# Kernel tuning notes

Measured on AMD Instinct MI355X. Metric: run time of the kernel, lower is better.

## Reference

```python
import jax, jax.numpy as jnp
import numpy as np

ENC_DIM = 512
B, T = 2048, 256
NUM_PARTS, PART_DIM, ATT_DIM, VOCAB = 64, 32, 128, 12


def _p(key, shape, scale=0.05):
    return jax.random.normal(key, shape, dtype=jnp.float32) * scale


def setup_inputs() -> dict:
    key = jax.random.key(0)
    ks = jax.random.split(key, 24)
    inp = {
        "img_features": jax.random.normal(ks[0], (B, 32, 8, 8), dtype=jnp.float32),
        "label": jax.random.normal(ks[1], (B, T, VOCAB), dtype=jnp.float32),
        # Attention params
        "Ww": _p(ks[2], (ATT_DIM, PART_DIM)), "Wb": _p(ks[3], (ATT_DIM,)),
        "Uw": _p(ks[4], (ATT_DIM, ENC_DIM)), "Ub": _p(ks[5], (ATT_DIM,)),
        "vw": _p(ks[6], (1, ATT_DIM)), "vb": _p(ks[7], (1,)),
        "betaw": _p(ks[8], (PART_DIM, ENC_DIM)), "betab": _p(ks[9], (PART_DIM,)),
        # init hidden params
        "ihw": _p(ks[10], (ENC_DIM, NUM_PARTS)), "ihb": _p(ks[11], (ENC_DIM,)),
        "icw": _p(ks[12], (ENC_DIM, NUM_PARTS)), "icb": _p(ks[13], (ENC_DIM,)),
        # LSTMCell params (PyTorch layout: [4*H, in] / [4*H, H])
        "W_ih": _p(ks[14], (4 * ENC_DIM, VOCAB + PART_DIM)),
        "W_hh": _p(ks[15], (4 * ENC_DIM, ENC_DIM)),
        "b_ih": _p(ks[16], (4 * ENC_DIM,)), "b_hh": _p(ks[17], (4 * ENC_DIM,)),
        # output fc
        "ow": _p(ks[18], (VOCAB, ENC_DIM)), "ob": _p(ks[19], (VOCAB,)),
    }
    return inp


def reference(img_features, label, Ww, Wb, Uw, Ub, vw, vb, betaw, betab,
              ihw, ihb, icw, icb, W_ih, W_hh, b_ih, b_hh, ow, ob):
    b = img_features.shape[0]
    feats = img_features.reshape(b, 32, -1)          # [B, 32, 64]
    parts = feats.transpose(0, 2, 1)                  # [B, 64, 32]
    # init hidden/cell from mean over channel dim (dim=1 in torch)
    avg = feats.mean(axis=1)                          # [B, 64]
    h0 = jnp.tanh(avg @ ihw.T + ihb)                  # [B, H]
    c0 = jnp.tanh(avg @ icw.T + icb)
    # W_s depends only on img features: hoist out of the loop (same math)
    Ws = parts @ Ww.T + Wb                            # [B, 64, 128]
    lab = label.transpose(1, 0, 2)                    # [T, B, 12]

    H = h0.shape[1]

    def step(carry, x_t):
        h, c = carry
        Uh = h @ Uw.T + Ub                            # [B, 128]
        att = jnp.tanh(Ws + Uh[:, None, :])           # [B, 64, 128]
        score = (att @ vw.T + vb)[..., 0]             # [B, 64]
        alpha = jax.nn.softmax(score, axis=1)
        ctx = jnp.einsum('bp,bpd->bd', alpha, parts)  # [B, 32]
        beta = jax.nn.sigmoid(h @ betaw.T + betab)
        ctx = ctx * beta
        inp = jnp.concatenate([x_t, ctx], axis=1)     # [B, 44]
        gates = inp @ W_ih.T + b_ih + h @ W_hh.T + b_hh
        i, f, g, o = jnp.split(gates, 4, axis=1)
        c2 = jax.nn.sigmoid(f) * c + jax.nn.sigmoid(i) * jnp.tanh(g)
        h2 = jax.nn.sigmoid(o) * jnp.tanh(c2)
        out = h2 @ ow.T + ob                          # [B, 12]
        return (h2, c2), (out, alpha)

    (_, _), (outs, alphas) = jax.lax.scan(step, (h0, c0), lab)
    output = jax.nn.log_softmax(outs, axis=-1).transpose(1, 0, 2)  # [B, T, 12]
    return output, alphas  # alphas: [T, B, 64] (stacked version of the list)
```

## Files before the change

kernel.cpp:

```cpp
#include <hip/hip_runtime.h>
#include <hip/hip_bf16.h>


typedef __attribute__((ext_vector_type(8))) short short8;
typedef __attribute__((ext_vector_type(4))) float floatx4;

#define DEV static __device__ __forceinline__
#define C2LE 2.885390082f
#define LOG2E 1.4426950409f
#define LN2 0.6931471806f

DEV unsigned short f2bf(float f) {
    unsigned int u = __float_as_uint(f);
    unsigned int r = (u + 0x7FFFu + ((u >> 16) & 1u)) >> 16;
    return (unsigned short)r;
}
DEV float bf2f(unsigned short u) { return __uint_as_float(((unsigned int)u) << 16); }
DEV float rcp_f(float x) { float r; asm("v_rcp_f32 %0, %1" : "=v"(r) : "v"(x)); return r; }
DEV float tanh_f(float x) { return 1.f - 2.f * rcp_f(1.f + exp2f(x * C2LE)); }
DEV float sigm(float x) { return rcp_f(1.f + exp2f(-x * LOG2E)); }

DEV void ldg16_sc(short8* d, const unsigned short* p) {
    asm volatile("global_load_dwordx4 %0, %1, off sc0 sc1" : "=v"(*d) : "v"(p));
}
DEV void stg2_sc(unsigned short* p, unsigned short v) {
    unsigned int vv = v;
    asm volatile("global_store_short %0, %1, off sc0 sc1" :: "v"(p), "v"(vv) : "memory");
}
DEV void st_flag(int* p, int v) {
    asm volatile("global_store_dword %0, %1, off sc0 sc1" :: "v"(p), "v"(v) : "memory");
}
DEV int ld_flag(const int* p) {
    int v;
    asm volatile("global_load_dword %0, %1, off sc0 sc1\n\ts_waitcnt vmcnt(0)"
                 : "=v"(v) : "v"(p) : "memory");
    return v;
}

#define OFF_XH0    ((size_t)0)
#define OFF_XH1    ((size_t)2359296)
#define OFF_C0     ((size_t)4718592)
#define OFF_PARTS  ((size_t)8912896)
#define OFF_WBIG   ((size_t)17301504)
#define OFF_WSMALL ((size_t)19660800)
#define OFF_WW2    ((size_t)19824640)
#define OFF_BIAS   ((size_t)19832832)
#define OFF_AVG    ((size_t)19841024)
#define OFF_FLAGS  ((size_t)20365312)

DEV void gbar(int* flags, int bk, int g16, int step) {
    asm volatile("s_waitcnt vmcnt(0)" ::: "memory");
    __syncthreads();
    if (threadIdx.x < 64) {
        int lane = threadIdx.x;
        if (lane == 0) st_flag(flags + bk * 32, step);
        for (;;) {
            int v = step;
            if (lane < 16) v = ld_flag(flags + (g16 + lane) * 32);
            if (__all(v >= step)) break;
            __builtin_amdgcn_s_sleep(1);
        }
    }
    __syncthreads();
}

__global__ void k_init(int* flags) {
    int i = blockIdx.x * 256 + threadIdx.x;
    if (i < 256 * 32) flags[i] = 0;
}

__global__ void k_avg(const float* __restrict__ img, float* __restrict__ avg) {
    int idx = blockIdx.x * 256 + threadIdx.x;
    int b = idx >> 6, p = idx & 63;
    const float* base = img + (size_t)b * 2048 + p;
    float s = 0.f;
#pragma unroll
    for (int k = 0; k < 32; ++k) s += base[k * 64];
    avg[idx] = s * (1.f / 32.f);
}

__global__ void k_prep(const float* __restrict__ Whh, const float* __restrict__ Wih,
                       const float* __restrict__ Uw, const float* __restrict__ betaw,
                       const float* __restrict__ Ww, const float* __restrict__ bih,
                       const float* __restrict__ bhh,
                       unsigned short* __restrict__ Wbig, unsigned short* __restrict__ Wsmall,
                       unsigned short* __restrict__ Ww2, float* __restrict__ bias_cat) {
    int p = blockIdx.x, tid = threadIdx.x;
    int g = p & 3, j = p >> 2, orig = g * 512 + j;
    for (int k = tid; k < 576; k += 256) {
        float v = 0.f;
        if (k < 512) v = Whh[(size_t)orig * 512 + k];
        else if (k < 556) v = Wih[(size_t)orig * 44 + (k - 512)];
        Wbig[(size_t)p * 576 + k] = f2bf(v);
    }
    if (p < 160) {
        for (int k = tid; k < 512; k += 256) {
            float v = (p < 128) ? Uw[(size_t)p * 512 + k] : betaw[(size_t)(p - 128) * 512 + k];
            Wsmall[(size_t)p * 512 + k] = f2bf(v);
        }
    }
    if (p < 128 && tid < 32) Ww2[p * 32 + tid] = f2bf(C2LE * Ww[p * 32 + tid]);
    if (tid == 0) bias_cat[orig] = bih[orig] + bhh[orig];
}

__global__ __launch_bounds__(512) void k_h0c0(const float* __restrict__ avg,
                                              const float* __restrict__ ihw, const float* __restrict__ ihb,
                                              const float* __restrict__ icw, const float* __restrict__ icb,
                                              unsigned short* __restrict__ xh0, unsigned short* __restrict__ xh1,
                                              float* __restrict__ c0) {
    __shared__ float avg_s[8][64];
    int b0 = blockIdx.x * 8, tid = threadIdx.x;
    for (int i = tid; i < 8 * 64; i += 512) avg_s[i >> 6][i & 63] = avg[b0 * 64 + i];
    __syncthreads();
    int j = tid;
    float w0[64];
#pragma unroll
    for (int p4 = 0; p4 < 16; ++p4) {
        float4 v = ((const float4*)(ihw + j * 64))[p4];
        w0[p4 * 4 + 0] = v.x; w0[p4 * 4 + 1] = v.y; w0[p4 * 4 + 2] = v.z; w0[p4 * 4 + 3] = v.w;
    }
    float bh = ihb[j];
#pragma unroll
    for (int bb = 0; bb < 8; ++bb) {
        float s = bh;
#pragma unroll
        for (int p = 0; p < 64; ++p) s += w0[p] * avg_s[bb][p];
        xh0[(size_t)(b0 + bb) * 576 + j] = f2bf(tanh_f(s));
        if (j < 20) {
            xh0[(size_t)(b0 + bb) * 576 + 556 + j] = 0;
            xh1[(size_t)(b0 + bb) * 576 + 556 + j] = 0;
        }
    }
#pragma unroll
    for (int p4 = 0; p4 < 16; ++p4) {
        float4 v = ((const float4*)(icw + j * 64))[p4];
        w0[p4 * 4 + 0] = v.x; w0[p4 * 4 + 1] = v.y; w0[p4 * 4 + 2] = v.z; w0[p4 * 4 + 3] = v.w;
    }
    float bc = icb[j];
#pragma unroll
    for (int bb = 0; bb < 8; ++bb) {
        float s = bc;
#pragma unroll
        for (int p = 0; p < 64; ++p) s += w0[p] * avg_s[bb][p];
        c0[(size_t)(b0 + bb) * 512 + j] = tanh_f(s);
    }
}

__global__ __launch_bounds__(256) void k_parts(const float* __restrict__ img,
                                               unsigned short* __restrict__ parts_bf) {
    __shared__ float pl[64][33];
    int b = blockIdx.x, tid = threadIdx.x;
    const float* ib = img + (size_t)b * 2048;
    for (int i = tid; i < 2048; i += 256) pl[i & 63][i >> 6] = ib[i];
    __syncthreads();
    for (int i = tid; i < 2048; i += 256)
        parts_bf[(size_t)b * 2048 + i] = f2bf(pl[i >> 5][i & 31]);
}

__global__ __launch_bounds__(512, 2) void k_scan(
    unsigned short* __restrict__ xh0, unsigned short* __restrict__ xh1,
    const float* __restrict__ c0,
    const unsigned short* __restrict__ parts_bf,
    const unsigned short* __restrict__ Wsmall, const unsigned short* __restrict__ Wbig,
    const unsigned short* __restrict__ Ww2, const float* __restrict__ bias_cat,
    const float* __restrict__ Ub, const float* __restrict__ betab, const float* __restrict__ Wb,
    const float* __restrict__ vw,
    const float* __restrict__ label, const float* __restrict__ ow, const float* __restrict__ ob,
    float* __restrict__ out_alpha, float* __restrict__ out_logits,
    int* __restrict__ flags)
{
    __shared__ unsigned short Ald[128 * 584];
    __shared__ float uh_l[8][160];
    __shared__ float al_l[8][64];
    __shared__ float vw2_l[128];
    __shared__ float bias_sl[128];

    const int tid = threadIdx.x, w = tid >> 6, lane = tid & 63;
    const int bk = blockIdx.x;
    const int mtile = bk >> 4, ntile = bk & 15;
    const int g16 = mtile * 16;
    const int wm = w >> 2, wn = w & 3;

    if (tid < 128) {
        vw2_l[tid] = -2.f * vw[tid];
        bias_sl[tid] = bias_cat[(tid >> 5) * 512 + ntile * 32 + (tid & 31)];
    }
    float creg[32];
#pragma unroll
    for (int mf = 0; mf < 4; ++mf)
#pragma unroll
        for (int nf = 0; nf < 2; ++nf)
#pragma unroll
            for (int r = 0; r < 4; ++r) {
                int b = mtile * 128 + wm * 64 + mf * 16 + (lane >> 4) * 4 + r;
                int j = ntile * 32 + wn * 8 + nf * 4 + (lane & 3);
                creg[(mf * 2 + nf) * 4 + r] = c0[(size_t)b * 512 + j];
            }
    __syncthreads();
    float vwsum = 0.f;
#pragma unroll
    for (int d = 0; d < 128; ++d) vwsum += vw2_l[d];
    vwsum *= -0.5f;

    auto stage_A = [&](const unsigned short* xin) {
#pragma unroll
        for (int half = 0; half < 2; ++half) {
            short8 tmp[9];
#pragma unroll
            for (int q = 0; q < 9; ++q) {
                int cid = tid + (half * 9 + q) * 512;
                int row = cid / 72, c16 = cid % 72;
                ldg16_sc(&tmp[q], xin + (size_t)(mtile * 128 + row) * 576 + c16 * 8);
            }
            asm volatile("s_waitcnt vmcnt(0)" ::: "memory");
            __builtin_amdgcn_sched_barrier(0);
#pragma unroll
            for (int q = 0; q < 9; ++q) {
                int cid = tid + (half * 9 + q) * 512;
                int row = cid / 72, c16 = cid % 72;
                *(short8*)&Ald[row * 584 + c16 * 8] = tmp[q];
            }
        }
    };

    auto phase1 = [&](unsigned short* xout) {
        const unsigned short* Bp = Wbig + (size_t)(ntile * 128 + wn * 32 + (lane & 15)) * 576 + (lane >> 4) * 8;
        const unsigned short* Ab = &Ald[(wm * 64 + (lane & 15)) * 584 + (lane >> 4) * 8];
        floatx4 acc[4][2] = {};
#pragma unroll 3
        for (int kk = 0; kk < 18; ++kk) {
            int k0 = kk * 32;
            short8 b0 = *(const short8*)(Bp + k0);
            short8 b1 = *(const short8*)(Bp + 16 * 576 + k0);
#pragma unroll
            for (int mf = 0; mf < 4; ++mf) {
                short8 a = *(const short8*)(Ab + mf * 16 * 584 + k0);
                acc[mf][0] = __builtin_amdgcn_mfma_f32_16x16x32_bf16(a, b0, acc[mf][0], 0, 0, 0);
                acc[mf][1] = __builtin_amdgcn_mfma_f32_16x16x32_bf16(a, b1, acc[mf][1], 0, 0, 0);
            }
        }
        int base = (lane & 48) | (4 * (lane & 3));
        int jl = wn * 8 + (lane & 3);
#pragma unroll
        for (int mf = 0; mf < 4; ++mf)
#pragma unroll
            for (int nf = 0; nf < 2; ++nf) {
#pragma unroll
                for (int r = 0; r < 4; ++r) {
                    float x = acc[mf][nf][r];
                    float g0 = __shfl(x, base + 0);
                    float g1 = __shfl(x, base + 1);
                    float g2 = __shfl(x, base + 2);
                    float g3 = __shfl(x, base + 3);
                    int jj = jl + nf * 4;
                    float gi = g0 + bias_sl[jj];
                    float gf = g1 + bias_sl[32 + jj];
                    float gg = g2 + bias_sl[64 + jj];
                    float go = g3 + bias_sl[96 + jj];
                    int ci = (mf * 2 + nf) * 4 + r;
                    float c2 = sigm(gf) * creg[ci] + sigm(gi) * tanh_f(gg);
                    creg[ci] = c2;
                    float h2 = sigm(go) * tanh_f(c2);
                    if (((lane >> 2) & 3) == 0) {
                        int bg = mtile * 128 + wm * 64 + mf * 16 + (lane >> 4) * 4 + r;
                        stg2_sc(xout + (size_t)bg * 576 + ntile * 32 + jj, f2bf(h2));
                    }
                }
            }
    };

    auto phase2 = [&](int tt, unsigned short* xb, bool do_head, bool do_attn) {
        {
            int row = tid >> 6, c16 = tid & 63;
            short8 tv;
            ldg16_sc(&tv, xb + (size_t)(bk * 8 + row) * 576 + c16 * 8);
            asm volatile("s_waitcnt vmcnt(0)" ::: "memory");
            __builtin_amdgcn_sched_barrier(0);
            *(short8*)&Ald[(ntile * 8 + row) * 584 + c16 * 8] = tv;
        }
        __syncthreads();
        int b = bk * 8 + w;
        if (do_head) {
            short8 hv = *(const short8*)&Ald[(ntile * 8 + w) * 584 + lane * 8];
            float hf[8];
#pragma unroll
            for (int j = 0; j < 8; ++j) hf[j] = bf2f((unsigned short)hv[j]);
            float ov[12];
#pragma unroll
            for (int v = 0; v < 12; ++v) {
                const float* owr = ow + v * 512 + lane * 8;
                float4 o0 = *(const float4*)owr;
                float4 o1 = *(const float4*)(owr + 4);
                float p = hf[0] * o0.x + hf[1] * o0.y + hf[2] * o0.z + hf[3] * o0.w
                        + hf[4] * o1.x + hf[5] * o1.y + hf[6] * o1.z + hf[7] * o1.w;
#pragma unroll
                for (int o = 32; o; o >>= 1) p += __shfl_xor(p, o);
                ov[v] = p + ob[v];
            }
            float mx = ov[0];
#pragma unroll
            for (int v = 1; v < 12; ++v) mx = fmaxf(mx, ov[v]);
            float ss = 0.f;
#pragma unroll
            for (int v = 0; v < 12; ++v) ss += exp2f((ov[v] - mx) * LOG2E);
            float lse = mx + log2f(ss) * LN2;
#pragma unroll
            for (int v = 0; v < 12; ++v)
                if (lane == v) out_logits[((size_t)b * 256 + (tt - 1)) * 12 + v] = ov[v] - lse;
        }
        if (do_attn && w < 5) {
            const unsigned short* Bp = Wsmall + (size_t)(w * 32 + (lane & 15)) * 512 + (lane >> 4) * 8;
            const unsigned short* Ab = &Ald[(ntile * 8 + (lane & 7)) * 584 + (lane >> 4) * 8];
            floatx4 u0 = {}, u1 = {};
#pragma unroll 4
            for (int k0 = 0; k0 < 512; k0 += 32) {
                short8 a = *(const short8*)(Ab + k0);
                u0 = __builtin_amdgcn_mfma_f32_16x16x32_bf16(a, *(const short8*)(Bp + k0), u0, 0, 0, 0);
                u1 = __builtin_amdgcn_mfma_f32_16x16x32_bf16(a, *(const short8*)(Bp + 16 * 512 + k0), u1, 0, 0, 0);
            }
            int r0 = (lane >> 4) * 4, cc = lane & 15;
            if (r0 < 8) {
#pragma unroll
                for (int q = 0; q < 2; ++q) {
                    int n = w * 32 + q * 16 + cc;
#pragma unroll
                    for (int r = 0; r < 4; ++r) {
                        float val = (q ? u1[r] : u0[r]);
                        uh_l[r0 + r][n] = (n < 128) ? C2LE * (val + Ub[n] + Wb[n])
                                                    : (val + betab[n - 128]);
                    }
                }
            }
        }
        __syncthreads();
        if (do_attn) {
            const unsigned short* pb = parts_bf + (size_t)b * 2048;
            short8 pa[4];
#pragma unroll
            for (int mt = 0; mt < 4; ++mt)
                pa[mt] = *(const short8*)(pb + ((lane & 15) + 16 * mt) * 32 + (lane >> 4) * 8);
            float sc[4][4] = {};
#pragma unroll
            for (int nt = 0; nt < 8; ++nt) {
                short8 wwf = *(const short8*)(Ww2 + (size_t)((lane & 15) + 16 * nt) * 32 + (lane >> 4) * 8);
                int d = nt * 16 + (lane & 15);
                float ud = uh_l[w][d];
                float v2 = vw2_l[d];
#pragma unroll
                for (int mt = 0; mt < 4; ++mt) {
                    floatx4 z = {};
                    floatx4 wsa = __builtin_amdgcn_mfma_f32_16x16x32_bf16(pa[mt], wwf, z, 0, 0, 0);
#pragma unroll
                    for (int r = 0; r < 4; ++r)
                        sc[mt][r] += v2 * rcp_f(1.f + exp2f(wsa[r] + ud));
                }
            }
            float mx = -1e30f;
#pragma unroll
            for (int mt = 0; mt < 4; ++mt)
#pragma unroll
                for (int r = 0; r < 4; ++r) {
                    float s = sc[mt][r];
                    s += __shfl_xor(s, 1); s += __shfl_xor(s, 2);
                    s += __shfl_xor(s, 4); s += __shfl_xor(s, 8);
                    s += vwsum;
                    sc[mt][r] = s;
                    mx = fmaxf(mx, s);
                }
            mx = fmaxf(mx, __shfl_xor(mx, 16));
            mx = fmaxf(mx, __shfl_xor(mx, 32));
            float ssum = 0.f;
            float av[4][4];
#pragma unroll
            for (int mt = 0; mt < 4; ++mt)
#pragma unroll
                for (int r = 0; r < 4; ++r) {
                    av[mt][r] = exp2f((sc[mt][r] - mx) * LOG2E);
                    ssum += av[mt][r];
                }
            ssum += __shfl_xor(ssum, 16);
            ssum += __shfl_xor(ssum, 32);
            float rs = rcp_f(ssum);
#pragma unroll
            for (int mt = 0; mt < 4; ++mt) {
                if ((lane & 15) == mt) {
                    float4 fv = make_float4(av[mt][0] * rs, av[mt][1] * rs, av[mt][2] * rs, av[mt][3] * rs);
                    int p0 = mt * 16 + (lane >> 4) * 4;
                    *(float4*)&out_alpha[((size_t)tt * 2048 + b) * 64 + p0] = fv;
                    *(float4*)&al_l[w][p0] = fv;
                }
            }
            int k = lane & 31, half = lane >> 5;
            float cp = 0.f;
#pragma unroll
            for (int p = 0; p < 32; ++p) {
                int pp = half * 32 + p;
                cp += al_l[w][pp] * bf2f(parts_bf[(size_t)b * 2048 + pp * 32 + k]);
            }
            cp += __shfl_xor(cp, 32);
            if (half == 0) {
                float beta = sigm(uh_l[w][128 + k]);
                stg2_sc(xb + (size_t)b * 576 + 524 + k, f2bf(cp * beta));
            }
            if (lane < 12)
                stg2_sc(xb + (size_t)b * 576 + 512 + lane, f2bf(label[((size_t)b * 256 + tt) * 12 + lane]));
        }
    };

    int bc = 0;
    phase2(0, xh0, false, true);
    gbar(flags, bk, g16, ++bc);
    for (int t = 0; t < 256; ++t) {
        const unsigned short* xin = (t & 1) ? xh1 : xh0;
        unsigned short* xout = (t & 1) ? xh0 : xh1;
        stage_A(xin);
        __syncthreads();
        phase1(xout);
        gbar(flags, bk, g16, ++bc);
        phase2(t + 1, xout, true, t < 255);
        if (t < 255) gbar(flags, bk, g16, ++bc);
    }
}

extern "C" void kernel_launch(void* const* d_in, const int* in_sizes, int n_in,
                              void* d_out, int out_size, void* d_ws, size_t ws_size,
                              hipStream_t stream) {
    const float* img   = (const float*)d_in[0];
    const float* label = (const float*)d_in[1];
    const float* Ww    = (const float*)d_in[2];
    const float* Wb    = (const float*)d_in[3];
    const float* Uw    = (const float*)d_in[4];
    const float* Ub    = (const float*)d_in[5];
    const float* vw    = (const float*)d_in[6];
    const float* betaw = (const float*)d_in[8];
    const float* betab = (const float*)d_in[9];
    const float* ihw   = (const float*)d_in[10];
    const float* ihb   = (const float*)d_in[11];
    const float* icw   = (const float*)d_in[12];
    const float* icb   = (const float*)d_in[13];
    const float* Wih   = (const float*)d_in[14];
    const float* Whh   = (const float*)d_in[15];
    const float* bih   = (const float*)d_in[16];
    const float* bhh   = (const float*)d_in[17];
    const float* ow    = (const float*)d_in[18];
    const float* ob    = (const float*)d_in[19];

    char* ws = (char*)d_ws;
    unsigned short* xh0      = (unsigned short*)(ws + OFF_XH0);
    unsigned short* xh1      = (unsigned short*)(ws + OFF_XH1);
    float*          c0       = (float*)(ws + OFF_C0);
    unsigned short* parts_bf = (unsigned short*)(ws + OFF_PARTS);
    unsigned short* Wbig     = (unsigned short*)(ws + OFF_WBIG);
    unsigned short* Wsmall   = (unsigned short*)(ws + OFF_WSMALL);
    unsigned short* Ww2      = (unsigned short*)(ws + OFF_WW2);
    float*          bias     = (float*)(ws + OFF_BIAS);
    float*          avg      = (float*)(ws + OFF_AVG);
    int*            flags    = (int*)(ws + OFF_FLAGS);

    float* out_logits = (float*)d_out;
    float* out_alpha  = out_logits + (size_t)2048 * 256 * 12;

    k_init<<<32, 256, 0, stream>>>(flags);
    k_avg<<<512, 256, 0, stream>>>(img, avg);
    k_prep<<<2048, 256, 0, stream>>>(Whh, Wih, Uw, betaw, Ww, bih, bhh, Wbig, Wsmall, Ww2, bias);
    k_h0c0<<<256, 512, 0, stream>>>(avg, ihw, ihb, icw, icb, xh0, xh1, c0);
    k_parts<<<2048, 256, 0, stream>>>(img, parts_bf);

    k_scan<<<256, 512, 0, stream>>>(xh0, xh1, c0, parts_bf, Wsmall, Wbig, Ww2, bias,
                                    Ub, betab, Wb, vw, label, ow, ob,
                                    out_alpha, out_logits, flags);
}
```

Before: 16.31 ms.

## Retile persistent LSTM scan into 4-block groups with single hidden buffer and LDS caching

Changes the scan tiling from 16 N-tiles per 128-row M-tile to 4 N-tiles per 32-row M-tile. Each inter-block barrier now waits on 4 peers instead of 16. The ping-pong hidden buffers are merged into one, and parts, the output weights and the biases are cached in LDS so they are not reloaded every step. Staging of peer rows is overlapped with the attention computation, and the h and context stores are packed into 8-byte writes. The trade-off is that each block now carries a heavier per-step GEMM (8 N-fragments per wave), and reusing a single buffer relies on carefully ordered barriers to avoid read/write races.

Result: faster. 15.22 ms (-6.7%).

```diff
diff --git a/kernel.cpp b/kernel.cpp
--- a/kernel.cpp
+++ b/kernel.cpp
@@ -4,6 +4,7 @@
 
 typedef __attribute__((ext_vector_type(8))) short short8;
 typedef __attribute__((ext_vector_type(4))) float floatx4;
+typedef __attribute__((ext_vector_type(2))) unsigned int uint2v;
 
 #define DEV static __device__ __forceinline__
 #define C2LE 2.885390082f
@@ -23,9 +24,8 @@
 DEV void ldg16_sc(short8* d, const unsigned short* p) {
     asm volatile("global_load_dwordx4 %0, %1, off sc0 sc1" : "=v"(*d) : "v"(p));
 }
-DEV void stg2_sc(unsigned short* p, unsigned short v) {
-    unsigned int vv = v;
-    asm volatile("global_store_short %0, %1, off sc0 sc1" :: "v"(p), "v"(vv) : "memory");
+DEV void stg8_sc(unsigned short* p, uint2v v) {
+    asm volatile("global_store_dwordx2 %0, %1, off sc0 sc1" :: "v"(p), "v"(v) : "memory");
 }
 DEV void st_flag(int* p, int v) {
     asm volatile("global_store_dword %0, %1, off sc0 sc1" :: "v"(p), "v"(v) : "memory");
@@ -36,27 +36,27 @@
                  : "=v"(v) : "v"(p) : "memory");
     return v;
 }
-
-#define OFF_XH0    ((size_t)0)
-#define OFF_XH1    ((size_t)2359296)
-#define OFF_C0     ((size_t)4718592)
-#define OFF_PARTS  ((size_t)8912896)
-#define OFF_WBIG   ((size_t)17301504)
-#define OFF_WSMALL ((size_t)19660800)
-#define OFF_WW2    ((size_t)19824640)
-#define OFF_BIAS   ((size_t)19832832)
-#define OFF_AVG    ((size_t)19841024)
-#define OFF_FLAGS  ((size_t)20365312)
-
-DEV void gbar(int* flags, int bk, int g16, int step) {
-    asm volatile("s_waitcnt vmcnt(0)" ::: "memory");
+DEV void waitv0() { asm volatile("s_waitcnt vmcnt(0)" ::: "memory"); }
+
+#define OFF_XH     ((size_t)0)
+#define OFF_C0     ((size_t)2359296)
+#define OFF_PARTS  ((size_t)6553600)
+#define OFF_WBIG   ((size_t)14942208)
+#define OFF_WSMALL ((size_t)17301504)
+#define OFF_WW2    ((size_t)17465344)
+#define OFF_BIAS   ((size_t)17473536)
+#define OFF_AVG    ((size_t)17481728)
+#define OFF_FLAGS  ((size_t)18006016)
+
+DEV void gbar(int* flags, int bk, int g4, int step) {
+    waitv0();
     __syncthreads();
     if (threadIdx.x < 64) {
         int lane = threadIdx.x;
         if (lane == 0) st_flag(flags + bk * 32, step);
         for (;;) {
             int v = step;
-            if (lane < 16) v = ld_flag(flags + (g16 + lane) * 32);
+            if (lane < 4) v = ld_flag(flags + (g4 + lane) * 32);
             if (__all(v >= step)) break;
             __builtin_amdgcn_s_sleep(1);
         }
@@ -106,8 +106,7 @@
 __global__ __launch_bounds__(512) void k_h0c0(const float* __restrict__ avg,
                                               const float* __restrict__ ihw, const float* __restrict__ ihb,
                                               const float* __restrict__ icw, const float* __restrict__ icb,
-                                              unsigned short* __restrict__ xh0, unsigned short* __restrict__ xh1,
-                                              float* __restrict__ c0) {
+                                              unsigned short* __restrict__ xh, float* __restrict__ c0) {
     __shared__ float avg_s[8][64];
     int b0 = blockIdx.x * 8, tid = threadIdx.x;
     for (int i = tid; i < 8 * 64; i += 512) avg_s[i >> 6][i & 63] = avg[b0 * 64 + i];
@@ -125,11 +124,8 @@
         float s = bh;
 #pragma unroll
         for (int p = 0; p < 64; ++p) s += w0[p] * avg_s[bb][p];
-        xh0[(size_t)(b0 + bb) * 576 + j] = f2bf(tanh_f(s));
-        if (j < 20) {
-            xh0[(size_t)(b0 + bb) * 576 + 556 + j] = 0;
-            xh1[(size_t)(b0 + bb) * 576 + 556 + j] = 0;
-        }
+        xh[(size_t)(b0 + bb) * 576 + j] = f2bf(tanh_f(s));
+        if (j < 20) xh[(size_t)(b0 + bb) * 576 + 556 + j] = 0;
     }
 #pragma unroll
     for (int p4 = 0; p4 < 16; ++p4) {
@@ -158,7 +154,7 @@
 }
 
 __global__ __launch_bounds__(512, 2) void k_scan(
-    unsigned short* __restrict__ xh0, unsigned short* __restrict__ xh1,
+    unsigned short* __restrict__ xh,
     const float* __restrict__ c0,
     const unsigned short* __restrict__ parts_bf,
     const unsigned short* __restrict__ Wsmall, const unsigned short* __restrict__ Wbig,
@@ -169,146 +165,69 @@
     float* __restrict__ out_alpha, float* __restrict__ out_logits,
     int* __restrict__ flags)
 {
-    __shared__ unsigned short Ald[128 * 584];
+    __shared__ unsigned short Ald[32 * 584];
+    __shared__ unsigned short parts_l[8][2304];
+    __shared__ unsigned short ow_l[12][512];
     __shared__ float uh_l[8][160];
     __shared__ float al_l[8][64];
+    __shared__ float bias_l[512];
+    __shared__ unsigned short xscr[8][48];
     __shared__ float vw2_l[128];
-    __shared__ float bias_sl[128];
+    __shared__ float obl[12];
 
     const int tid = threadIdx.x, w = tid >> 6, lane = tid & 63;
     const int bk = blockIdx.x;
-    const int mtile = bk >> 4, ntile = bk & 15;
-    const int g16 = mtile * 16;
+    const int mtile = bk >> 2, ntile = bk & 3;
+    const int g4 = bk & ~3;
     const int wm = w >> 2, wn = w & 3;
 
-    if (tid < 128) {
-        vw2_l[tid] = -2.f * vw[tid];
-        bias_sl[tid] = bias_cat[(tid >> 5) * 512 + ntile * 32 + (tid & 31)];
+    if (tid < 128) vw2_l[tid] = -2.f * vw[tid];
+    if (tid < 12) obl[tid] = ob[tid];
+    if (tid < 512) {
+        int g = tid >> 7, jl = tid & 127;
+        bias_l[tid] = bias_cat[g * 512 + ntile * 128 + jl];
+    }
+    for (int i = tid; i < 12 * 512; i += 512) ow_l[i >> 9][i & 511] = f2bf(ow[i]);
+    {
+        int row = tid >> 6, p = tid & 63;
+        const short8* src = (const short8*)(parts_bf + (size_t)(bk * 8 + row) * 2048 + p * 32);
+        short8* dst = (short8*)&parts_l[row][p * 36];
+        dst[0] = src[0]; dst[1] = src[1]; dst[2] = src[2]; dst[3] = src[3];
     }
     float creg[32];
 #pragma unroll
-    for (int mf = 0; mf < 4; ++mf)
-#pragma unroll
-        for (int nf = 0; nf < 2; ++nf)
-#pragma unroll
-            for (int r = 0; r < 4; ++r) {
-                int b = mtile * 128 + wm * 64 + mf * 16 + (lane >> 4) * 4 + r;
-                int j = ntile * 32 + wn * 8 + nf * 4 + (lane & 3);
-                creg[(mf * 2 + nf) * 4 + r] = c0[(size_t)b * 512 + j];
-            }
+    for (int nf = 0; nf < 8; ++nf)
+#pragma unroll
+        for (int r = 0; r < 4; ++r) {
+            int b = mtile * 32 + wm * 16 + (lane >> 4) * 4 + r;
+            int j = ntile * 128 + wn * 32 + nf * 4 + (lane & 3);
+            creg[nf * 4 + r] = c0[(size_t)b * 512 + j];
+        }
+    {
+        short8 tv[4];
+#pragma unroll
+        for (int q = 0; q < 4; ++q) {
+            int cid = tid + q * 512;
+            int row = cid >> 6, c16 = cid & 63;
+            ldg16_sc(&tv[q], xh + (size_t)(mtile * 32 + row) * 576 + c16 * 8);
+        }
+        waitv0();
+        __builtin_amdgcn_sched_barrier(0);
+#pragma unroll
+        for (int q = 0; q < 4; ++q) {
+            int cid = tid + q * 512;
+            int row = cid >> 6, c16 = cid & 63;
+            *(short8*)&Ald[row * 584 + c16 * 8] = tv[q];
+        }
+    }
     __syncthreads();
     float vwsum = 0.f;
 #pragma unroll
     for (int d = 0; d < 128; ++d) vwsum += vw2_l[d];
     vwsum *= -0.5f;
 
-    auto stage_A = [&](const unsigned short* xin) {
-#pragma unroll
-        for (int half = 0; half < 2; ++half) {
-            short8 tmp[9];
-#pragma unroll
-            for (int q = 0; q < 9; ++q) {
-                int cid = tid + (half * 9 + q) * 512;
-                int row = cid / 72, c16 = cid % 72;
-                ldg16_sc(&tmp[q], xin + (size_t)(mtile * 128 + row) * 576 + c16 * 8);
-            }
-            asm volatile("s_waitcnt vmcnt(0)" ::: "memory");
-            __builtin_amdgcn_sched_barrier(0);
-#pragma unroll
-            for (int q = 0; q < 9; ++q) {
-                int cid = tid + (half * 9 + q) * 512;
-                int row = cid / 72, c16 = cid % 72;
-                *(short8*)&Ald[row * 584 + c16 * 8] = tmp[q];
-            }
-        }
-    };
-
-    auto phase1 = [&](unsigned short* xout) {
-        const unsigned short* Bp = Wbig + (size_t)(ntile * 128 + wn * 32 + (lane & 15)) * 576 + (lane >> 4) * 8;
-        const unsigned short* Ab = &Ald[(wm * 64 + (lane & 15)) * 584 + (lane >> 4) * 8];
-        floatx4 acc[4][2] = {};
-#pragma unroll 3
-        for (int kk = 0; kk < 18; ++kk) {
-            int k0 = kk * 32;
-            short8 b0 = *(const short8*)(Bp + k0);
-            short8 b1 = *(const short8*)(Bp + 16 * 576 + k0);
-#pragma unroll
-            for (int mf = 0; mf < 4; ++mf) {
-                short8 a = *(const short8*)(Ab + mf * 16 * 584 + k0);
-                acc[mf][0] = __builtin_amdgcn_mfma_f32_16x16x32_bf16(a, b0, acc[mf][0], 0, 0, 0);
-                acc[mf][1] = __builtin_amdgcn_mfma_f32_16x16x32_bf16(a, b1, acc[mf][1], 0, 0, 0);
-            }
-        }
-        int base = (lane & 48) | (4 * (lane & 3));
-        int jl = wn * 8 + (lane & 3);
-#pragma unroll
-        for (int mf = 0; mf < 4; ++mf)
-#pragma unroll
-            for (int nf = 0; nf < 2; ++nf) {
-#pragma unroll
-                for (int r = 0; r < 4; ++r) {
-                    float x = acc[mf][nf][r];
-                    float g0 = __shfl(x, base + 0);
-                    float g1 = __shfl(x, base + 1);
-                    float g2 = __shfl(x, base + 2);
-                    float g3 = __shfl(x, base + 3);
-                    int jj = jl + nf * 4;
-                    float gi = g0 + bias_sl[jj];
-                    float gf = g1 + bias_sl[32 + jj];
-                    float gg = g2 + bias_sl[64 + jj];
-                    float go = g3 + bias_sl[96 + jj];
-                    int ci = (mf * 2 + nf) * 4 + r;
-                    float c2 = sigm(gf) * creg[ci] + sigm(gi) * tanh_f(gg);
-                    creg[ci] = c2;
-                    float h2 = sigm(go) * tanh_f(c2);
-                    if (((lane >> 2) & 3) == 0) {
-                        int bg = mtile * 128 + wm * 64 + mf * 16 + (lane >> 4) * 4 + r;
-                        stg2_sc(xout + (size_t)bg * 576 + ntile * 32 + jj, f2bf(h2));
-                    }
-                }
-            }
-    };
-
-    auto phase2 = [&](int tt, unsigned short* xb, bool do_head, bool do_attn) {
-        {
-            int row = tid >> 6, c16 = tid & 63;
-            short8 tv;
-            ldg16_sc(&tv, xb + (size_t)(bk * 8 + row) * 576 + c16 * 8);
-            asm volatile("s_waitcnt vmcnt(0)" ::: "memory");
-            __builtin_amdgcn_sched_barrier(0);
-            *(short8*)&Ald[(ntile * 8 + row) * 584 + c16 * 8] = tv;
-        }
-        __syncthreads();
-        int b = bk * 8 + w;
-        if (do_head) {
-            short8 hv = *(const short8*)&Ald[(ntile * 8 + w) * 584 + lane * 8];
-            float hf[8];
-#pragma unroll
-            for (int j = 0; j < 8; ++j) hf[j] = bf2f((unsigned short)hv[j]);
-            float ov[12];
-#pragma unroll
-            for (int v = 0; v < 12; ++v) {
-                const float* owr = ow + v * 512 + lane * 8;
-                float4 o0 = *(const float4*)owr;
-                float4 o1 = *(const float4*)(owr + 4);
-                float p = hf[0] * o0.x + hf[1] * o0.y + hf[2] * o0.z + hf[3] * o0.w
-                        + hf[4] * o1.x + hf[5] * o1.y + hf[6] * o1.z + hf[7] * o1.w;
-#pragma unroll
-                for (int o = 32; o; o >>= 1) p += __shfl_xor(p, o);
-                ov[v] = p + ob[v];
-            }
-            float mx = ov[0];
-#pragma unroll
-            for (int v = 1; v < 12; ++v) mx = fmaxf(mx, ov[v]);
-            float ss = 0.f;
-#pragma unroll
-            for (int v = 0; v < 12; ++v) ss += exp2f((ov[v] - mx) * LOG2E);
-            float lse = mx + log2f(ss) * LN2;
-#pragma unroll
-            for (int v = 0; v < 12; ++v)
-                if (lane == v) out_logits[((size_t)b * 256 + (tt - 1)) * 12 + v] = ov[v] - lse;
-        }
-        if (do_attn && w < 5) {
+    auto do_uh = [&]() {
+        if (w < 5) {
             const unsigned short* Bp = Wsmall + (size_t)(w * 32 + (lane & 15)) * 512 + (lane >> 4) * 8;
             const unsigned short* Ab = &Ald[(ntile * 8 + (lane & 7)) * 584 + (lane >> 4) * 8];
             floatx4 u0 = {}, u1 = {};
@@ -332,93 +251,213 @@
                 }
             }
         }
+    };
+
+    auto do_head = [&](int tt) {
+        int b = bk * 8 + w;
+        short8 hv = *(const short8*)&Ald[(ntile * 8 + w) * 584 + lane * 8];
+        float hf[8];
+#pragma unroll
+        for (int j = 0; j < 8; ++j) hf[j] = bf2f((unsigned short)hv[j]);
+        float ov[12];
+#pragma unroll
+        for (int v = 0; v < 12; ++v) {
+            short8 wv = *(const short8*)&ow_l[v][lane * 8];
+            float p = 0.f;
+#pragma unroll
+            for (int j = 0; j < 8; ++j) p += hf[j] * bf2f((unsigned short)wv[j]);
+#pragma unroll
+            for (int o = 32; o; o >>= 1) p += __shfl_xor(p, o);
+            ov[v] = p + obl[v];
+        }
+        float mx = ov[0];
+#pragma unroll
+        for (int v = 1; v < 12; ++v) mx = fmaxf(mx, ov[v]);
+        float ss = 0.f;
+#pragma unroll
+        for (int v = 0; v < 12; ++v) ss += exp2f((ov[v] - mx) * LOG2E);
+        float lse = mx + log2f(ss) * LN2;
+#pragma unroll
+        for (int v = 0; v < 12; ++v)
+            if (lane == v) out_logits[((size_t)b * 256 + tt) * 12 + v] = ov[v] - lse;
+    };
+
+    auto do_attn = [&](int tt) {
+        int b = bk * 8 + w;
+        short8 pa[4];
+#pragma unroll
+        for (int mt = 0; mt < 4; ++mt)
+            pa[mt] = *(const short8*)&parts_l[w][(mt * 16 + (lane & 15)) * 36 + (lane >> 4) * 8];
+        float sc[4][4] = {};
+#pragma unroll
+        for (int nt = 0; nt < 8; ++nt) {
+            short8 wwf = *(const short8*)(Ww2 + (size_t)((lane & 15) + 16 * nt) * 32 + (lane >> 4) * 8);
+            int d = nt * 16 + (lane & 15);
+            float ud = uh_l[w][d];
+            float v2 = vw2_l[d];
+#pragma unroll
+            for (int mt = 0; mt < 4; ++mt) {
+                floatx4 z = {};
+                floatx4 wsa = __builtin_amdgcn_mfma_f32_16x16x32_bf16(pa[mt], wwf, z, 0, 0, 0);
+#pragma unroll
+                for (int r = 0; r < 4; ++r)
+                    sc[mt][r] += v2 * rcp_f(1.f + exp2f(wsa[r] + ud));
+            }
+        }
+        float mx = -1e30f;
+#pragma unroll
+        for (int mt = 0; mt < 4; ++mt)
+#pragma unroll
+            for (int r = 0; r < 4; ++r) {
+                float s = sc[mt][r];
+                s += __shfl_xor(s, 1); s += __shfl_xor(s, 2);
+                s += __shfl_xor(s, 4); s += __shfl_xor(s, 8);
+                s += vwsum;
+                sc[mt][r] = s;
+                mx = fmaxf(mx, s);
+            }
+        mx = fmaxf(mx, __shfl_xor(mx, 16));
+        mx = fmaxf(mx, __shfl_xor(mx, 32));
+        float ssum = 0.f;
+        float av[4][4];
+#pragma unroll
+        for (int mt = 0; mt < 4; ++mt)
+#pragma unroll
+            for (int r = 0; r < 4; ++r) {
+                av[mt][r] = exp2f((sc[mt][r] - mx) * LOG2E);
+                ssum += av[mt][r];
+            }
+        ssum += __shfl_xor(ssum, 16);
+        ssum += __shfl_xor(ssum, 32);
+        float rs = rcp_f(ssum);
+#pragma unroll
+        for (int mt = 0; mt < 4; ++mt) {
+            if ((lane & 15) == mt) {
+                float4 fv = make_float4(av[mt][0] * rs, av[mt][1] * rs, av[mt][2] * rs, av[mt][3] * rs);
+                int p0 = mt * 16 + (lane >> 4) * 4;
+                *(float4*)&out_alpha[((size_t)tt * 2048 + b) * 64 + p0] = fv;
+                *(float4*)&al_l[w][p0] = fv;
+            }
+        }
+        int k = lane & 31, half = lane >> 5;
+        float cp = 0.f;
+#pragma unroll
+        for (int p = 0; p < 32; ++p) {
+            int pp = half * 32 + p;
+            cp += al_l[w][pp] * bf2f(parts_l[w][pp * 36 + k]);
+        }
+        cp += __shfl_xor(cp, 32);
+        if (half == 0) xscr[w][12 + k] = f2bf(cp * sigm(uh_l[w][128 + k]));
+        if (lane < 12) xscr[w][lane] = f2bf(label[((size_t)b * 256 + tt) * 12 + lane]);
+        if (lane < 11) {
+            uint2v v = *(const uint2v*)&xscr[w][lane * 4];
+            stg8_sc(xh + (size_t)b * 576 + 512 + lane * 4, v);
+        }
+    };
+
+    auto phase1 = [&]() {
+        const unsigned short* Bp = Wbig + (size_t)(ntile * 512 + wn * 128 + (lane & 15)) * 576 + (lane >> 4) * 8;
+        const unsigned short* Ab = &Ald[(wm * 16 + (lane & 15)) * 584 + (lane >> 4) * 8];
+        floatx4 acc[8] = {};
+#pragma unroll 2
+        for (int kk = 0; kk < 18; ++kk) {
+            int k0 = kk * 32;
+            short8 a = *(const short8*)(Ab + k0);
+#pragma unroll
+            for (int nf = 0; nf < 8; ++nf) {
+                short8 bv = *(const short8*)(Bp + (size_t)nf * 9216 + k0);
+                acc[nf] = __builtin_amdgcn_mfma_f32_16x16x32_bf16(a, bv, acc[nf], 0, 0, 0);
+            }
+        }
+        int base = (lane & 48) | ((lane & 3) * 4);
+#pragma unroll
+        for (int nf = 0; nf < 8; ++nf) {
+            int jl = wn * 32 + nf * 4 + (lane & 3);
+            float bi = bias_l[jl], bfv = bias_l[128 + jl], bg = bias_l[256 + jl], bo = bias_l[384 + jl];
+#pragma unroll
+            for (int r = 0; r < 4; ++r) {
+                float x = acc[nf][r];
+                float g0 = __shfl(x, base + 0);
+                float g1 = __shfl(x, base + 1);
+                float g2 = __shfl(x, base + 2);
+                float g3 = __shfl(x, base + 3);
+                int ci = nf * 4 + r;
+                float c2 = sigm(g1 + bfv) * creg[ci] + sigm(g0 + bi) * tanh_f(g2 + bg);
+                creg[ci] = c2;
+                float h2 = sigm(g3 + bo) * tanh_f(c2);
+                unsigned int hv = f2bf(h2);
+                unsigned int o1 = (unsigned int)__shfl_xor((int)hv, 1) & 0xFFFFu;
+                unsigned int pair = (lane & 1) ? (o1 | (hv << 16)) : (hv | (o1 << 16));
+                unsigned int o2 = (unsigned int)__shfl_xor((int)pair, 2);
+                if ((lane & 15) == 0) {
+                    int row = mtile * 32 + wm * 16 + (lane >> 4) * 4 + r;
+                    uint2v v; v[0] = pair; v[1] = o2;
+                    stg8_sc(xh + (size_t)row * 576 + ntile * 128 + wn * 32 + nf * 4, v);
+                }
+            }
+        }
+    };
+
+    do_uh();
+    __syncthreads();
+    do_attn(0);
+    int bc = 0;
+    gbar(flags, bk, g4, ++bc);
+    if (tid < 256) {
+        short8 tv;
+        int row = tid >> 3, c16 = tid & 7;
+        ldg16_sc(&tv, xh + (size_t)(mtile * 32 + row) * 576 + 512 + c16 * 8);
+        waitv0();
+        __builtin_amdgcn_sched_barrier(0);
+        *(short8*)&Ald[row * 584 + 512 + c16 * 8] = tv;
+    }
+    __syncthreads();
+
+    for (int t = 0; t < 256; ++t) {
+        phase1();
+        gbar(flags, bk, g4, ++bc);
+        {
+            short8 tv;
+            int row = tid >> 6, c16 = tid & 63;
+            ldg16_sc(&tv, xh + (size_t)(bk * 8 + row) * 576 + c16 * 8);
+            waitv0();
+            __builtin_amdgcn_sched_barrier(0);
+            *(short8*)&Ald[(ntile * 8 + row) * 584 + c16 * 8] = tv;
+        }
         __syncthreads();
-        if (do_attn) {
-            const unsigned short* pb = parts_bf + (size_t)b * 2048;
-            short8 pa[4];
-#pragma unroll
-            for (int mt = 0; mt < 4; ++mt)
-                pa[mt] = *(const short8*)(pb + ((lane & 15) + 16 * mt) * 32 + (lane >> 4) * 8);
-            float sc[4][4] = {};
-#pragma unroll
-            for (int nt = 0; nt < 8; ++nt) {
-                short8 wwf = *(const short8*)(Ww2 + (size_t)((lane & 15) + 16 * nt) * 32 + (lane >> 4) * 8);
-                int d = nt * 16 + (lane & 15);
-                float ud = uh_l[w][d];
-                float v2 = vw2_l[d];
-#pragma unroll
-                for (int mt = 0; mt < 4; ++mt) {
-                    floatx4 z = {};
-                    floatx4 wsa = __builtin_amdgcn_mfma_f32_16x16x32_bf16(pa[mt], wwf, z, 0, 0, 0);
-#pragma unroll
-                    for (int r = 0; r < 4; ++r)
-                        sc[mt][r] += v2 * rcp_f(1.f + exp2f(wsa[r] + ud));
-                }
-            }
-            float mx = -1e30f;
-#pragma unroll
-            for (int mt = 0; mt < 4; ++mt)
-#pragma unroll
-                for (int r = 0; r < 4; ++r) {
-                    float s = sc[mt][r];
-                    s += __shfl_xor(s, 1); s += __shfl_xor(s, 2);
-                    s += __shfl_xor(s, 4); s += __shfl_xor(s, 8);
-                    s += vwsum;
-                    sc[mt][r] = s;
-                    mx = fmaxf(mx, s);
-                }
-            mx = fmaxf(mx, __shfl_xor(mx, 16));
-            mx = fmaxf(mx, __shfl_xor(mx, 32));
-            float ssum = 0.f;
-            float av[4][4];
-#pragma unroll
-            for (int mt = 0; mt < 4; ++mt)
-#pragma unroll
-                for (int r = 0; r < 4; ++r) {
-                    av[mt][r] = exp2f((sc[mt][r] - mx) * LOG2E);
-                    ssum += av[mt][r];
-                }
-            ssum += __shfl_xor(ssum, 16);
-            ssum += __shfl_xor(ssum, 32);
-            float rs = rcp_f(ssum);
-#pragma unroll
-            for (int mt = 0; mt < 4; ++mt) {
-                if ((lane & 15) == mt) {
-                    float4 fv = make_float4(av[mt][0] * rs, av[mt][1] * rs, av[mt][2] * rs, av[mt][3] * rs);
-                    int p0 = mt * 16 + (lane >> 4) * 4;
-                    *(float4*)&out_alpha[((size_t)tt * 2048 + b) * 64 + p0] = fv;
-                    *(float4*)&al_l[w][p0] = fv;
-                }
-            }
-            int k = lane & 31, half = lane >> 5;
-            float cp = 0.f;
-#pragma unroll
-            for (int p = 0; p < 32; ++p) {
-                int pp = half * 32 + p;
-                cp += al_l[w][pp] * bf2f(parts_bf[(size_t)b * 2048 + pp * 32 + k]);
-            }
-            cp += __shfl_xor(cp, 32);
-            if (half == 0) {
-                float beta = sigm(uh_l[w][128 + k]);
-                stg2_sc(xb + (size_t)b * 576 + 524 + k, f2bf(cp * beta));
-            }
-            if (lane < 12)
-                stg2_sc(xb + (size_t)b * 576 + 512 + lane, f2bf(label[((size_t)b * 256 + tt) * 12 + lane]));
-        }
-    };
-
-    int bc = 0;
-    phase2(0, xh0, false, true);
-    gbar(flags, bk, g16, ++bc);
-    for (int t = 0; t < 256; ++t) {
-        const unsigned short* xin = (t & 1) ? xh1 : xh0;
-        unsigned short* xout = (t & 1) ? xh0 : xh1;
-        stage_A(xin);
+        do_head(t);
+        if (t < 255) do_uh();
         __syncthreads();
-        phase1(xout);
-        gbar(flags, bk, g16, ++bc);
-        phase2(t + 1, xout, true, t < 255);
-        if (t < 255) gbar(flags, bk, g16, ++bc);
+        if (t < 255) {
+            short8 s24[3];
+#pragma unroll
+            for (int q = 0; q < 3; ++q) {
+                int cid = tid + q * 512;
+                int r24 = cid >> 6, c16 = cid & 63;
+                int lr = (r24 < ntile * 8) ? r24 : r24 + 8;
+                ldg16_sc(&s24[q], xh + (size_t)(mtile * 32 + lr) * 576 + c16 * 8);
+            }
+            do_attn(t + 1);
+            waitv0();
+            __builtin_amdgcn_sched_barrier(0);
+#pragma unroll
+            for (int q = 0; q < 3; ++q) {
+                int cid = tid + q * 512;
+                int r24 = cid >> 6, c16 = cid & 63;
+                int lr = (r24 < ntile * 8) ? r24 : r24 + 8;
+                *(short8*)&Ald[lr * 584 + c16 * 8] = s24[q];
+            }
+            gbar(flags, bk, g4, ++bc);
+            if (tid < 256) {
+                short8 tv;
+                int row = tid >> 3, c16 = tid & 7;
+                ldg16_sc(&tv, xh + (size_t)(mtile * 32 + row) * 576 + 512 + c16 * 8);
+                waitv0();
+                __builtin_amdgcn_sched_barrier(0);
+                *(short8*)&Ald[row * 584 + 512 + c16 * 8] = tv;
+            }
+            __syncthreads();
+        }
     }
 }
 
@@ -446,8 +485,7 @@
     const float* ob    = (const float*)d_in[19];
 
     char* ws = (char*)d_ws;
-    unsigned short* xh0      = (unsigned short*)(ws + OFF_XH0);
-    unsigned short* xh1      = (unsigned short*)(ws + OFF_XH1);
+    unsigned short* xh       = (unsigned short*)(ws + OFF_XH);
     float*          c0       = (float*)(ws + OFF_C0);
     unsigned short* parts_bf = (unsigned short*)(ws + OFF_PARTS);
     unsigned short* Wbig     = (unsigned short*)(ws + OFF_WBIG);
@@ -463,10 +501,10 @@
     k_init<<<32, 256, 0, stream>>>(flags);
     k_avg<<<512, 256, 0, stream>>>(img, avg);
     k_prep<<<2048, 256, 0, stream>>>(Whh, Wih, Uw, betaw, Ww, bih, bhh, Wbig, Wsmall, Ww2, bias);
-    k_h0c0<<<256, 512, 0, stream>>>(avg, ihw, ihb, icw, icb, xh0, xh1, c0);
+    k_h0c0<<<256, 512, 0, stream>>>(avg, ihw, ihb, icw, icb, xh, c0);
     k_parts<<<2048, 256, 0, stream>>>(img, parts_bf);
 
-    k_scan<<<256, 512, 0, stream>>>(xh0, xh1, c0, parts_bf, Wsmall, Wbig, Ww2, bias,
+    k_scan<<<256, 512, 0, stream>>>(xh, c0, parts_bf, Wsmall, Wbig, Ww2, bias,
                                     Ub, betab, Wb, vw, label, ow, ob,
                                     out_alpha, out_logits, flags);
 }
```
